# Performance work log

Measured on AMD Instinct MI355X. Metric: run time of the kernel, lower is better.

Reference implementation:

```python
import jax, jax.numpy as jnp
import numpy as np


def setup_inputs() -> dict:
    key = jax.random.key(0)
    ks = jax.random.split(key, 8)
    N, E = 10000, 160000
    IN, OUT, TC = 512, 512, 256
    x = jax.random.normal(ks[0], (N, IN), dtype=jnp.float32)
    t_emb = jax.random.normal(ks[1], (TC,), dtype=jnp.float32)
    edge_index = jax.random.randint(ks[2], (2, E), 0, N, dtype=jnp.int64)
    # GCNConv weight (glorot-ish scale) and bias
    W = jax.random.normal(ks[3], (IN, OUT), dtype=jnp.float32) / np.sqrt(IN)
    b = jnp.zeros((OUT,), dtype=jnp.float32)
    # time_proj Linear(TC, OUT)
    Wt = jax.random.normal(ks[4], (TC, OUT), dtype=jnp.float32) / np.sqrt(TC)
    bt = jnp.zeros((OUT,), dtype=jnp.float32)
    return {"x": x, "t_emb": t_emb, "edge_index": edge_index,
            "W": W, "b": b, "Wt": Wt, "bt": bt}


def _gcn_conv(x, edge_index, W, b):
    # PyG GCNConv: add self-loops, symmetric normalization, xW, scatter-add, +bias
    N = x.shape[0]
    loops = jnp.arange(N, dtype=edge_index.dtype)
    src = jnp.concatenate([edge_index[0], loops])  # [E+N]
    dst = jnp.concatenate([edge_index[1], loops])
    deg = jax.ops.segment_sum(jnp.ones_like(dst, dtype=x.dtype), dst,
                              num_segments=N)  # in-degree incl. self-loop
    dinv = jnp.where(deg > 0, jax.lax.rsqrt(deg), 0.0)
    norm = dinv[src] * dinv[dst]  # [E+N]
    xw = x @ W  # [N, OUT] - transform before gather (fewer FLOPs on edges)
    msgs = norm[:, None] * xw[src]  # [E+N, OUT]
    out = jax.ops.segment_sum(msgs, dst, num_segments=N)
    return out + b


def reference(x, t_emb, edge_index, W, b, Wt, bt):
    h = _gcn_conv(x, edge_index, W, b)          # [N, OUT]
    time_emb = t_emb @ Wt + bt                   # [OUT] (1-D t_emb branch)
    return h + time_emb
```

## Files before the change

kernel.cpp:

```cpp
#include <hip/hip_runtime.h>

#define OUTC 512
#define INC 512
#define TPB 256
#define CAP 96

typedef __bf16 bf16x8 __attribute__((ext_vector_type(8)));
typedef float f32x4 __attribute__((ext_vector_type(4)));

typedef __attribute__((address_space(1))) const unsigned char as1_u8;
typedef __attribute__((address_space(3))) unsigned char as3_u8;
static __device__ __forceinline__ void gload16(const void* g, void* l) {
    __builtin_amdgcn_global_load_lds((as1_u8*)g, (as3_u8*)l, 16, 0, 0);
}

static __device__ __forceinline__ unsigned short f2bf(float f) {
    unsigned u = __float_as_uint(f);
    unsigned r = u + 0x7fffu + ((u >> 16) & 1u);
    return (unsigned short)(r >> 16);
}
static __device__ __forceinline__ float bflo(unsigned r) { return __uint_as_float(r << 16); }
static __device__ __forceinline__ float bfhi(unsigned r) { return __uint_as_float(r & 0xffff0000u); }
static __device__ __forceinline__ void acc8s(float* a, uint4 v, float n) {
    a[0] += n * bflo(v.x); a[1] += n * bfhi(v.x);
    a[2] += n * bflo(v.y); a[3] += n * bfhi(v.y);
    a[4] += n * bflo(v.z); a[5] += n * bfhi(v.z);
    a[6] += n * bflo(v.w); a[7] += n * bfhi(v.w);
}

__global__ __launch_bounds__(256) void k_prep(const float* __restrict__ x,
                                              const float* __restrict__ W,
                                              const float* __restrict__ t_emb,
                                              const float* __restrict__ Wt,
                                              const float* __restrict__ bt,
                                              const float* __restrict__ b,
                                              int* __restrict__ counts,
                                              unsigned short* __restrict__ xb,
                                              unsigned short* __restrict__ wtb,
                                              float* __restrict__ temb,
                                              int ZB, int XBB,
                                              int M, int Mpad, int TC) {
    __shared__ float smem[32 * 33];
    int bid = blockIdx.x;
    if (bid < ZB) {
        int i = bid * 256 + threadIdx.x;
        if (i < M) counts[i] = 0;
    } else if (bid < ZB + XBB) {
        int idx = (bid - ZB) * 256 + threadIdx.x;
        int row = idx >> 6;
        int kg = (idx & 63) * 8;
        ushort4 h0 = make_ushort4(0, 0, 0, 0), h1 = make_ushort4(0, 0, 0, 0);
        if (row < M) {
            float4 v0 = *(const float4*)(x + (size_t)row * INC + kg);
            float4 v1 = *(const float4*)(x + (size_t)row * INC + kg + 4);
            h0 = make_ushort4(f2bf(v0.x), f2bf(v0.y), f2bf(v0.z), f2bf(v0.w));
            h1 = make_ushort4(f2bf(v1.x), f2bf(v1.y), f2bf(v1.z), f2bf(v1.w));
        }
        *(ushort4*)(xb + (size_t)row * INC + kg) = h0;
        *(ushort4*)(xb + (size_t)row * INC + kg + 4) = h1;
    } else if (bid < ZB + XBB + 256) {
        int b2 = bid - (ZB + XBB);
        int bk = (b2 & 15) * 32, bn = (b2 >> 4) * 32;
        int tx = threadIdx.x & 31, ty = threadIdx.x >> 5;
        for (int r = ty; r < 32; r += 8)
            smem[r * 33 + tx] = W[(size_t)(bk + r) * OUTC + bn + tx];
        __syncthreads();
        for (int r = ty; r < 32; r += 8)
            wtb[(size_t)(bn + r) * INC + bk + tx] = f2bf(smem[tx * 33 + r]);
    } else {
        int j = bid - (ZB + XBB + 256);
        int t = threadIdx.x;
        float p = 0.0f;
        for (int k = t; k < TC; k += 256) p += t_emb[k] * Wt[(size_t)k * OUTC + j];
        smem[t] = p;
        __syncthreads();
        for (int s = 128; s > 0; s >>= 1) {
            if (t < s) smem[t] += smem[t + s];
            __syncthreads();
        }
        if (t == 0) temb[j] = smem[0] + bt[j] + b[j];
    }
}

__global__ __launch_bounds__(256) void k_ag(const unsigned short* __restrict__ xb,
                                            const unsigned short* __restrict__ wtb,
                                            unsigned short* __restrict__ xwb,
                                            const int* __restrict__ src,
                                            const int* __restrict__ dst,
                                            int* __restrict__ counts,
                                            int* __restrict__ slots,
                                            int E, int Mpad) {
    __shared__ unsigned short lsA[2][128 * 64];
    __shared__ unsigned short lsB[2][128 * 64];

    const int bid = blockIdx.x;
    const int tid = threadIdx.x;
    const int GB = (Mpad / 128) * (OUTC / 128);

    if (bid >= GB) {
        int e = (bid - GB) * 256 + tid;
        if (e < E) {
            int s = src[e];
            int d = dst[e];
            int pos = atomicAdd(&counts[d], 1);
            if (pos < CAP) slots[(size_t)d * CAP + pos] = s;
        }
        return;
    }

    const int n0 = (bid & 3) * 128;
    const int m0 = (bid >> 2) * 128;
    const int lane = tid & 63;
    const int wave = tid >> 6;
    const int wr = (wave >> 1) * 64;
    const int wc = (wave & 1) * 64;
    const int l15 = lane & 15;
    const int qb = lane >> 4;

    const int l8r = lane >> 3;
    const int swb = ((lane & 7) ^ l8r) << 4;

    const unsigned char* gA[4];
    const unsigned char* gB[4];
#pragma unroll
    for (int i = 0; i < 4; ++i) {
        int c = wave * 4 + i;
        int row = c * 8 + l8r;
        gA[i] = (const unsigned char*)(xb + (size_t)(m0 + row) * INC) + swb;
        gB[i] = (const unsigned char*)(wtb + (size_t)(n0 + row) * INC) + swb;
    }

    f32x4 acc[4][4];
#pragma unroll
    for (int m = 0; m < 4; ++m)
#pragma unroll
        for (int n = 0; n < 4; ++n)
            acc[m][n] = (f32x4){0.f, 0.f, 0.f, 0.f};

    unsigned short* pa = &lsA[0][0];
    unsigned short* pb = &lsB[0][0];
    unsigned short* qa = &lsA[1][0];
    unsigned short* qbf = &lsB[1][0];

#define STAGE(dA, dB, kb)                                                    \
    {                                                                        \
        _Pragma("unroll")                                                    \
        for (int i = 0; i < 4; ++i) {                                        \
            int c = wave * 4 + i;                                            \
            gload16(gA[i] + (kb) * 2, (unsigned char*)(dA) + c * 1024);      \
            gload16(gB[i] + (kb) * 2, (unsigned char*)(dB) + c * 1024);      \
        }                                                                    \
    }

    STAGE(pa, pb, 0);
    __syncthreads();

    for (int t = 0; t < INC / 64; ++t) {
        if (t < INC / 64 - 1) STAGE(qa, qbf, (t + 1) * 64);

#pragma unroll
        for (int kc = 0; kc < 64; kc += 32) {
            const int q = (kc >> 3) + qb;
            bf16x8 af[4], bv[4];
#pragma unroll
            for (int m = 0; m < 4; ++m) {
                int row = wr + m * 16 + l15;
                af[m] = *(const bf16x8*)((const unsigned char*)pa + row * 128 +
                                         ((q ^ (row & 7)) << 4));
            }
#pragma unroll
            for (int n = 0; n < 4; ++n) {
                int row = wc + n * 16 + l15;
                bv[n] = *(const bf16x8*)((const unsigned char*)pb + row * 128 +
                                         ((q ^ (row & 7)) << 4));
            }
#pragma unroll
            for (int m = 0; m < 4; ++m)
#pragma unroll
                for (int n = 0; n < 4; ++n)
                    acc[m][n] = __builtin_amdgcn_mfma_f32_16x16x32_bf16(af[m], bv[n], acc[m][n], 0, 0, 0);
        }

        __syncthreads();
        unsigned short* tmp;
        tmp = pa; pa = qa; qa = tmp;
        tmp = pb; pb = qbf; qbf = tmp;
    }
#undef STAGE

    const int rbase = (lane >> 4) * 4;
#pragma unroll
    for (int m = 0; m < 4; ++m)
#pragma unroll
        for (int n = 0; n < 4; ++n) {
            int gcol = n0 + wc + n * 16 + l15;
#pragma unroll
            for (int r = 0; r < 4; ++r) {
                int grow = m0 + wr + m * 16 + rbase + r;
                xwb[(size_t)grow * OUTC + gcol] = f2bf(acc[m][n][r]);
            }
        }
}

__global__ __launch_bounds__(256) void k_gather(const int* __restrict__ slots,
                                                const int* __restrict__ counts,
                                                const unsigned short* __restrict__ xwb,
                                                const float* __restrict__ temb,
                                                float* __restrict__ out, int N) {
    __shared__ float red[4 * 512];
    const int node = blockIdx.x;
    const int tid = threadIdx.x;
    const int lane = tid & 63;
    const int wave = tid >> 6;

    const int deg = counts[node];
    const int dc = deg < CAP ? deg : CAP;
    const int* sp = slots + (size_t)node * CAP;

    float a[8] = {0.f, 0.f, 0.f, 0.f, 0.f, 0.f, 0.f, 0.f};
    int i = wave;
    for (; i + 4 < dc; i += 8) {
        int s0 = sp[i];
        int s1 = sp[i + 4];
        uint4 v0 = *(const uint4*)(xwb + (size_t)s0 * OUTC + lane * 8);
        uint4 v1 = *(const uint4*)(xwb + (size_t)s1 * OUTC + lane * 8);
        float n0 = rsqrtf((float)counts[s0] + 1.0f);
        float n1 = rsqrtf((float)counts[s1] + 1.0f);
        acc8s(a, v0, n0);
        acc8s(a, v1, n1);
    }
    if (i < dc) {
        int s0 = sp[i];
        uint4 v0 = *(const uint4*)(xwb + (size_t)s0 * OUTC + lane * 8);
        acc8s(a, v0, rsqrtf((float)counts[s0] + 1.0f));
    }

    float* rw = red + wave * 512;
#pragma unroll
    for (int k = 0; k < 8; ++k) rw[k * 64 + lane] = a[k];
    __syncthreads();

    const float di = rsqrtf((float)deg + 1.0f);
    const int c0 = tid * 2;
    const int c1 = c0 + 1;
    unsigned selfw = *(const unsigned*)(xwb + (size_t)node * OUTC + c0);
    float2 tv = *(const float2*)(temb + c0);
    float e0 = 0.f, e1 = 0.f;
#pragma unroll
    for (int w = 0; w < 4; ++w) {
        e0 += red[w * 512 + (c0 & 7) * 64 + (c0 >> 3)];
        e1 += red[w * 512 + (c1 & 7) * 64 + (c1 >> 3)];
    }
    float2 o;
    o.x = di * (e0 + di * bflo(selfw)) + tv.x;
    o.y = di * (e1 + di * bfhi(selfw)) + tv.y;
    *(float2*)(out + (size_t)node * OUTC + c0) = o;
}

extern "C" void kernel_launch(void* const* d_in, const int* in_sizes, int n_in,
                              void* d_out, int out_size, void* d_ws, size_t ws_size,
                              hipStream_t stream) {
    const float* x     = (const float*)d_in[0];
    const float* t_emb = (const float*)d_in[1];
    const int*   ei    = (const int*)d_in[2];
    const float* W     = (const float*)d_in[3];
    const float* b     = (const float*)d_in[4];
    const float* Wt    = (const float*)d_in[5];
    const float* bt    = (const float*)d_in[6];
    float* out = (float*)d_out;

    const int N  = in_sizes[0] / INC;
    const int E  = in_sizes[2] / 2;
    const int TC = in_sizes[1];
    const int Mpad = (N + 127) & ~127;

    char* ws = (char*)d_ws;
    size_t off = 0;
    unsigned short* xb  = (unsigned short*)(ws + off); off += (size_t)Mpad * INC * 2;
    unsigned short* xwb = (unsigned short*)(ws + off); off += (size_t)Mpad * OUTC * 2;
    unsigned short* wtb = (unsigned short*)(ws + off); off += (size_t)INC * OUTC * 2;
    int* counts = (int*)(ws + off);        off += ((size_t)N * 4 + 255) & ~(size_t)255;
    int* slots  = (int*)(ws + off);        off += ((size_t)N * CAP * 4 + 255) & ~(size_t)255;
    float* temb = (float*)(ws + off);      off += OUTC * 4;

    const int* srcIdx = ei;
    const int* dstIdx = ei + E;

    const int ZB  = (N + 255) / 256;
    const int XBB = Mpad * (INC / 8) / 256;
    const int GB  = (Mpad / 128) * (OUTC / 128);
    const int SB  = (E + 255) / 256;

    k_prep<<<ZB + XBB + 256 + OUTC, TPB, 0, stream>>>(x, W, t_emb, Wt, bt, b,
                                                      counts, xb, wtb, temb,
                                                      ZB, XBB, N, Mpad, TC);
    k_ag<<<GB + SB, TPB, 0, stream>>>(xb, wtb, xwb, srcIdx, dstIdx,
                                      counts, slots, E, Mpad);

    k_gather<<<N, TPB, 0, stream>>>(slots, counts, xwb, temb, out, N);
}
```

Before: 123.7 us.

## Assign one wavefront per node in gather kernel, dropping LDS reduction

The gather kernel used to spread each node's neighbour list across four wavefronts and then combine their partial sums through shared memory and a block barrier. Now each wavefront handles one whole node, with four nodes per block, so there is no LDS reduction and no __syncthreads. The self-loop term is folded into the same accumulator, and the output is written with float4 stores. Each node's neighbour loads now run serially inside a single wave, which lowers memory-level parallelism per node.

New measurement: 125.5 us. About the same (+1.4%).

```diff
diff --git a/kernel.cpp b/kernel.cpp
--- a/kernel.cpp
+++ b/kernel.cpp
@@ -207,23 +207,23 @@
                                                 const unsigned short* __restrict__ xwb,
                                                 const float* __restrict__ temb,
                                                 float* __restrict__ out, int N) {
-    __shared__ float red[4 * 512];
-    const int node = blockIdx.x;
-    const int tid = threadIdx.x;
-    const int lane = tid & 63;
-    const int wave = tid >> 6;
+    const int wave = threadIdx.x >> 6;
+    const int node = blockIdx.x * 4 + wave;
+    if (node >= N) return;
+    const int lane = threadIdx.x & 63;
+    const int c8 = lane * 8;
 
     const int deg = counts[node];
     const int dc = deg < CAP ? deg : CAP;
     const int* sp = slots + (size_t)node * CAP;
 
     float a[8] = {0.f, 0.f, 0.f, 0.f, 0.f, 0.f, 0.f, 0.f};
-    int i = wave;
-    for (; i + 4 < dc; i += 8) {
+    int i = 0;
+    for (; i + 2 <= dc; i += 2) {
         int s0 = sp[i];
-        int s1 = sp[i + 4];
-        uint4 v0 = *(const uint4*)(xwb + (size_t)s0 * OUTC + lane * 8);
-        uint4 v1 = *(const uint4*)(xwb + (size_t)s1 * OUTC + lane * 8);
+        int s1 = sp[i + 1];
+        uint4 v0 = *(const uint4*)(xwb + (size_t)s0 * OUTC + c8);
+        uint4 v1 = *(const uint4*)(xwb + (size_t)s1 * OUTC + c8);
         float n0 = rsqrtf((float)counts[s0] + 1.0f);
         float n1 = rsqrtf((float)counts[s1] + 1.0f);
         acc8s(a, v0, n0);
@@ -231,30 +231,25 @@
     }
     if (i < dc) {
         int s0 = sp[i];
-        uint4 v0 = *(const uint4*)(xwb + (size_t)s0 * OUTC + lane * 8);
+        uint4 v0 = *(const uint4*)(xwb + (size_t)s0 * OUTC + c8);
         acc8s(a, v0, rsqrtf((float)counts[s0] + 1.0f));
     }
 
-    float* rw = red + wave * 512;
-#pragma unroll
-    for (int k = 0; k < 8; ++k) rw[k * 64 + lane] = a[k];
-    __syncthreads();
-
     const float di = rsqrtf((float)deg + 1.0f);
-    const int c0 = tid * 2;
-    const int c1 = c0 + 1;
-    unsigned selfw = *(const unsigned*)(xwb + (size_t)node * OUTC + c0);
-    float2 tv = *(const float2*)(temb + c0);
-    float e0 = 0.f, e1 = 0.f;
-#pragma unroll
-    for (int w = 0; w < 4; ++w) {
-        e0 += red[w * 512 + (c0 & 7) * 64 + (c0 >> 3)];
-        e1 += red[w * 512 + (c1 & 7) * 64 + (c1 >> 3)];
-    }
-    float2 o;
-    o.x = di * (e0 + di * bflo(selfw)) + tv.x;
-    o.y = di * (e1 + di * bfhi(selfw)) + tv.y;
-    *(float2*)(out + (size_t)node * OUTC + c0) = o;
+    {
+        uint4 vs = *(const uint4*)(xwb + (size_t)node * OUTC + c8);
+        acc8s(a, vs, di);
+    }
+    float4 t0 = *(const float4*)(temb + c8);
+    float4 t1 = *(const float4*)(temb + c8 + 4);
+    float4 o0, o1;
+    o0.x = di * a[0] + t0.x; o0.y = di * a[1] + t0.y;
+    o0.z = di * a[2] + t0.z; o0.w = di * a[3] + t0.w;
+    o1.x = di * a[4] + t1.x; o1.y = di * a[5] + t1.y;
+    o1.z = di * a[6] + t1.z; o1.w = di * a[7] + t1.w;
+    float* op = out + (size_t)node * OUTC + c8;
+    *(float4*)(op) = o0;
+    *(float4*)(op + 4) = o1;
 }
 
 extern "C" void kernel_launch(void* const* d_in, const int* in_sizes, int n_in,
@@ -297,5 +292,5 @@
     k_ag<<<GB + SB, TPB, 0, stream>>>(xb, wtb, xwb, srcIdx, dstIdx,
                                       counts, slots, E, Mpad);
 
-    k_gather<<<N, TPB, 0, stream>>>(slots, counts, xwb, temb, out, N);
-}
+    k_gather<<<(N + 3) / 4, TPB, 0, stream>>>(slots, counts, xwb, temb, out, N);
+}
```
